# Kernel optimization log

Measured on AMD Instinct MI355X. Metric: run time of the kernel, lower is better.

Reference implementation:

```python
import jax, jax.numpy as jnp
import numpy as np

K = 121          # kernel_size
C = 3            # channels
PAD = (K - 1) // 2  # 60, replicate padding so output matches input spatial size


def setup_inputs() -> dict:
    key = jax.random.key(0)
    k1, k2 = jax.random.split(key)
    x = jax.random.normal(k1, (8, C, 512, 512), dtype=jnp.float32)
    sigma = jax.random.uniform(k2, (), dtype=jnp.float32)
    return {"x": x, "sigma": sigma}


def _gaussian_kernel(sigma):
    # sigma -> sigma*8 + 16, variance = sigma**2 (as in torch forward)
    s = sigma * 8.0 + 16.0
    variance = s * s
    coord = jnp.arange(K, dtype=jnp.float32) - (K - 1) / 2.0  # centered coords
    diff = -(coord[:, None] ** 2 + coord[None, :] ** 2)       # [K,K], -((x-m)^2+(y-m)^2)
    kern = jnp.exp(diff / (2.0 * variance))
    # the 1/(2*pi*variance) prefactor cancels under normalization
    kern = kern / jnp.sum(kern)
    return kern


def reference(x, sigma):
    kern = _gaussian_kernel(sigma)
    # depthwise weights: [out_ch=C, in_ch/groups=1, K, K]
    w = jnp.broadcast_to(kern[None, None, :, :], (C, 1, K, K))
    # replicate padding (torch 'replicate' == jnp 'edge')
    xp = jnp.pad(x, ((0, 0), (0, 0), (PAD, PAD), (PAD, PAD)), mode="edge")
    out = jax.lax.conv_general_dilated(
        xp, w,
        window_strides=(1, 1),
        padding="VALID",
        dimension_numbers=("NCHW", "OIHW", "NCHW"),
        feature_group_count=C,
    )
    return out
```

## Files before the change

kernel.cpp:

```cpp
#include <hip/hip_runtime.h>


#define HH    512
#define WW    512
#define PLANE (512 * 512)
#define NIMG  24
#define SROW  960

__device__ __forceinline__ int qla(int s) {
    return 10 * (s >> 2) + 2 * (s & 3);
}

__device__ __forceinline__ void make_weights(const float* __restrict__ sigma,
                                             float* __restrict__ wlds, int tid) {
    const float s = sigma[0] * 8.0f + 16.0f;
    const float inv2v = 1.0f / (2.0f * s * s);
    const int lane = tid & 63;
    const float c1 = (float)lane - 60.0f;
    float sum = __expf(-c1 * c1 * inv2v);
    if (lane + 64 <= 120) {
        const float c2 = (float)(lane + 64) - 60.0f;
        sum += __expf(-c2 * c2 * inv2v);
    }
    #pragma unroll
    for (int off = 1; off < 64; off <<= 1) sum += __shfl_xor(sum, off);
    if (tid < 128) {
        float g = 0.0f;
        if (tid <= 120) {
            const float c = (float)tid - 60.0f;
            g = __expf(-c * c * inv2v);
        }
        wlds[tid] = g / sum;
    }
}

#define V_OCT(CUR, NXT, KO)                                               \
    { *(float4*)&wq[0] = *(const float4*)&wlds[(KO) * 8];                 \
      *(float4*)&wq[4] = *(const float4*)&wlds[(KO) * 8 + 4];             \
      _Pragma("unroll")                                                   \
      for (int ki = 0; ki < 8; ++ki) {                                    \
          int rr = r0 - 52 + (KO) * 8 + ki;                               \
          rr = rr < 0 ? 0 : (rr > HH - 1 ? HH - 1 : rr);                  \
          NXT[ki] = *(const float2*)&src[(size_t)rr * WW];                \
          const float wk = wq[ki];                                        \
          _Pragma("unroll")                                               \
          for (int j = 0; j < 8; ++j) {                                   \
              const int idx = ki + j;                                     \
              const float2 v = (idx < 8) ? CUR[idx] : NXT[idx - 8];       \
              vac[j].x += wk * v.x; vac[j].y += wk * v.y;                 \
          }                                                               \
      }                                                                   \
    }

#define LOADW(DST, MB)                                                    \
    { const int F = 20 * (L + (MB));                                      \
      const float4 A = *(const float4*)&bs[F];                            \
      const float4 Bq = *(const float4*)&bs[F + 4];                       \
      const float4 Cq = *(const float4*)&bs[F + 10];                      \
      const float4 Dq = *(const float4*)&bs[F + 14];                      \
      DST[0] = make_float2(A.x, A.y);   DST[1] = make_float2(A.z, A.w);   \
      DST[2] = make_float2(Bq.x, Bq.y); DST[3] = make_float2(Bq.z, Bq.w); \
      DST[4] = make_float2(Cq.x, Cq.y); DST[5] = make_float2(Cq.z, Cq.w); \
      DST[6] = make_float2(Dq.x, Dq.y); DST[7] = make_float2(Dq.z, Dq.w); }

#define H_OCT(CUR, NXT, KO)                                               \
    { LOADW(NXT, (KO) + 1)                                                \
      *(float4*)&wq[0] = *(const float4*)&wlds[(KO) * 8];                 \
      *(float4*)&wq[4] = *(const float4*)&wlds[(KO) * 8 + 4];             \
      _Pragma("unroll")                                                   \
      for (int ki = 0; ki < 8; ++ki) {                                    \
          const float wk = wq[ki];                                        \
          _Pragma("unroll")                                               \
          for (int j = 0; j < 8; ++j) {                                   \
              const int idx = ki + j;                                     \
              const float2 v = (idx < 8) ? CUR[idx] : NXT[idx - 8];       \
              hac[j].x += wk * v.x; hac[j].y += wk * v.y;                 \
          }                                                               \
      }                                                                   \
    }

__global__ __launch_bounds__(256, 5) void blur_fused(
        const float* __restrict__ x, const float* __restrict__ sigma,
        float* __restrict__ out) {
    __shared__ float sm[8 * SROW];
    __shared__ float wlds[128];
    const int tid = threadIdx.x;

    const int lid   = blockIdx.x + gridDim.x * blockIdx.y;
    const int tile  = (lid & 7) * 192 + (lid >> 3);
    const int r0    = (tile & 63) * 8;
    const int plane = tile >> 6;

    const int c0 = tid * 2;
    const float* __restrict__ src = x + (size_t)plane * PLANE + c0;

    float2 wa[8], wb[8], vac[8];
    float  wq[8];
    #pragma unroll
    for (int m = 0; m < 8; ++m) {
        int rr = r0 - 60 + m;
        rr = rr < 0 ? 0 : rr;
        wa[m] = *(const float2*)&src[(size_t)rr * WW];
    }
    make_weights(sigma, wlds, tid);
    #pragma unroll
    for (int j = 0; j < 8; ++j) vac[j] = make_float2(0.f, 0.f);
    __syncthreads();

    #pragma unroll 1
    for (int ko = 0; ko < 16; ko += 2) {
        V_OCT(wa, wb, ko)
        V_OCT(wb, wa, ko + 1)
    }

    {
        const int laX0 = qla(c0 + 60), laX1 = qla(c0 + 61);
        const int laY0 = qla(c0 - 196) + 1, laY1 = qla(c0 - 195) + 1;
        #pragma unroll
        for (int j = 0; j < 8; ++j) {
            float* rp = sm + j * SROW;
            if (c0 < 324) { rp[laX0] = vac[j].x; rp[laX1] = vac[j].y; }
            if (c0 >= 196) { rp[laY0] = vac[j].x; rp[laY1] = vac[j].y; }
        }
    }
    if (tid < 64) {
        #pragma unroll
        for (int j = 0; j < 8; ++j) {
            const float lv = __shfl(vac[j].x, 0);
            if (tid < 60) sm[j * SROW + qla(tid)] = lv;
        }
    } else if (tid >= 192) {
        const int l = tid & 63;
        #pragma unroll
        for (int j = 0; j < 8; ++j) {
            const float rv = __shfl(vac[j].y, 63);
            sm[j * SROW + qla(316 + l) + 1] = rv;
            if (l < 4) sm[j * SROW + qla(380 + l) + 1] = rv;
        }
    }
    __syncthreads();

    const int r = tid >> 5;
    const int L = tid & 31;
    const float* __restrict__ bs = sm + r * SROW;

    float2 ha[8], hb[8], hac[8];
    #pragma unroll
    for (int j = 0; j < 8; ++j) hac[j] = make_float2(0.f, 0.f);

    LOADW(ha, 0)

    #pragma unroll 1
    for (int ko = 0; ko < 16; ko += 2) {
        H_OCT(ha, hb, ko)
        H_OCT(hb, ha, ko + 1)
    }

    float* __restrict__ dst = out + (size_t)plane * PLANE
                                  + (size_t)(r0 + r) * WW + L * 8;
    *(float4*)(dst)       = make_float4(hac[0].x, hac[1].x, hac[2].x, hac[3].x);
    *(float4*)(dst + 4)   = make_float4(hac[4].x, hac[5].x, hac[6].x, hac[7].x);
    *(float4*)(dst + 256) = make_float4(hac[0].y, hac[1].y, hac[2].y, hac[3].y);
    *(float4*)(dst + 260) = make_float4(hac[4].y, hac[5].y, hac[6].y, hac[7].y);
}

extern "C" void kernel_launch(void* const* d_in, const int* in_sizes, int n_in,
                              void* d_out, int out_size, void* d_ws, size_t ws_size,
                              hipStream_t stream) {
    const float* x     = (const float*)d_in[0];
    const float* sigma = (const float*)d_in[1];
    float* out = (float*)d_out;
    blur_fused<<<dim3(HH / 8, NIMG), dim3(256), 0, stream>>>(x, sigma, out);
}
```

Baseline: 119.6 us.

## Use packed FP32 FMA and triple-buffer row/column windows for deeper prefetch

Replaces scalar FMAs with inline v_pk_fma_f32 on duplicated float2 weights, which halves the FMA instruction count in both vertical and horizontal passes. Adds a third register buffer so loads run two octets ahead of use, giving more latency hiding. Occupancy hint drops from 5 to 4 blocks per CU to make room for the extra registers. Weights in LDS are stored as float2 pairs, doubling weight LDS traffic, and the shared buffer is padded.

```diff
diff --git a/kernel.cpp b/kernel.cpp
--- a/kernel.cpp
+++ b/kernel.cpp
@@ -12,7 +12,7 @@
 }
 
 __device__ __forceinline__ void make_weights(const float* __restrict__ sigma,
-                                             float* __restrict__ wlds, int tid) {
+                                             float2* __restrict__ wlds2, int tid) {
     const float s = sigma[0] * 8.0f + 16.0f;
     const float inv2v = 1.0f / (2.0f * s * s);
     const int lane = tid & 63;
@@ -30,24 +30,36 @@
             const float c = (float)tid - 60.0f;
             g = __expf(-c * c * inv2v);
         }
-        wlds[tid] = g / sum;
+        const float gn = g / sum;
+        wlds2[tid] = make_float2(gn, gn);
     }
 }
 
-#define V_OCT(CUR, NXT, KO)                                               \
-    { *(float4*)&wq[0] = *(const float4*)&wlds[(KO) * 8];                 \
-      *(float4*)&wq[4] = *(const float4*)&wlds[(KO) * 8 + 4];             \
+#define LOADWQ(KO)                                                        \
+    *(float4*)&wq2[0] = *(const float4*)&wlds2[(KO) * 8];                 \
+    *(float4*)&wq2[2] = *(const float4*)&wlds2[(KO) * 8 + 2];             \
+    *(float4*)&wq2[4] = *(const float4*)&wlds2[(KO) * 8 + 4];             \
+    *(float4*)&wq2[6] = *(const float4*)&wlds2[(KO) * 8 + 6];
+
+#define PKFMA(ACC, V, W)                                                  \
+    asm("v_pk_fma_f32 %0, %1, %2, %0" : "+v"(ACC) : "v"(V), "v"(W));
+
+#define V_OCT(W0, W1, W2, KO)                                             \
+    { _Pragma("unroll")                                                   \
+      for (int ki = 0; ki < 8; ++ki) {                                    \
+          int rr = r0 - 60 + ((KO) + 2) * 8 + ki;                         \
+          rr = rr < 0 ? 0 : (rr > HH - 1 ? HH - 1 : rr);                  \
+          W2[ki] = *(const float2*)&src[(size_t)rr * WW];                 \
+      }                                                                   \
+      LOADWQ(KO)                                                          \
       _Pragma("unroll")                                                   \
       for (int ki = 0; ki < 8; ++ki) {                                    \
-          int rr = r0 - 52 + (KO) * 8 + ki;                               \
-          rr = rr < 0 ? 0 : (rr > HH - 1 ? HH - 1 : rr);                  \
-          NXT[ki] = *(const float2*)&src[(size_t)rr * WW];                \
-          const float wk = wq[ki];                                        \
+          const float2 wk2 = wq2[ki];                                     \
           _Pragma("unroll")                                               \
           for (int j = 0; j < 8; ++j) {                                   \
               const int idx = ki + j;                                     \
-              const float2 v = (idx < 8) ? CUR[idx] : NXT[idx - 8];       \
-              vac[j].x += wk * v.x; vac[j].y += wk * v.y;                 \
+              const float2 v = (idx < 8) ? W0[idx] : W1[idx - 8];         \
+              PKFMA(vac[j], v, wk2)                                       \
           }                                                               \
       }                                                                   \
     }
@@ -63,27 +75,26 @@
       DST[4] = make_float2(Cq.x, Cq.y); DST[5] = make_float2(Cq.z, Cq.w); \
       DST[6] = make_float2(Dq.x, Dq.y); DST[7] = make_float2(Dq.z, Dq.w); }
 
-#define H_OCT(CUR, NXT, KO)                                               \
-    { LOADW(NXT, (KO) + 1)                                                \
-      *(float4*)&wq[0] = *(const float4*)&wlds[(KO) * 8];                 \
-      *(float4*)&wq[4] = *(const float4*)&wlds[(KO) * 8 + 4];             \
+#define H_OCT(W0, W1, W2, KO)                                             \
+    { LOADW(W2, (KO) + 2)                                                 \
+      LOADWQ(KO)                                                          \
       _Pragma("unroll")                                                   \
       for (int ki = 0; ki < 8; ++ki) {                                    \
-          const float wk = wq[ki];                                        \
+          const float2 wk2 = wq2[ki];                                     \
           _Pragma("unroll")                                               \
           for (int j = 0; j < 8; ++j) {                                   \
               const int idx = ki + j;                                     \
-              const float2 v = (idx < 8) ? CUR[idx] : NXT[idx - 8];       \
-              hac[j].x += wk * v.x; hac[j].y += wk * v.y;                 \
+              const float2 v = (idx < 8) ? W0[idx] : W1[idx - 8];         \
+              PKFMA(hac[j], v, wk2)                                       \
           }                                                               \
       }                                                                   \
     }
 
-__global__ __launch_bounds__(256, 5) void blur_fused(
+__global__ __launch_bounds__(256, 4) void blur_fused(
         const float* __restrict__ x, const float* __restrict__ sigma,
         float* __restrict__ out) {
-    __shared__ float sm[8 * SROW];
-    __shared__ float wlds[128];
+    __shared__ float  sm[8 * SROW + 40];
+    __shared__ float2 wlds2[128];
     const int tid = threadIdx.x;
 
     const int lid   = blockIdx.x + gridDim.x * blockIdx.y;
@@ -94,24 +105,31 @@
     const int c0 = tid * 2;
     const float* __restrict__ src = x + (size_t)plane * PLANE + c0;
 
-    float2 wa[8], wb[8], vac[8];
-    float  wq[8];
+    float2 Wa[8], Wb[8], Wc[8], vac[8], wq2[8];
     #pragma unroll
     for (int m = 0; m < 8; ++m) {
         int rr = r0 - 60 + m;
         rr = rr < 0 ? 0 : rr;
-        wa[m] = *(const float2*)&src[(size_t)rr * WW];
+        Wa[m] = *(const float2*)&src[(size_t)rr * WW];
     }
-    make_weights(sigma, wlds, tid);
+    #pragma unroll
+    for (int m = 0; m < 8; ++m) {
+        int rr = r0 - 52 + m;
+        rr = rr < 0 ? 0 : rr;
+        Wb[m] = *(const float2*)&src[(size_t)rr * WW];
+    }
+    make_weights(sigma, wlds2, tid);
     #pragma unroll
     for (int j = 0; j < 8; ++j) vac[j] = make_float2(0.f, 0.f);
     __syncthreads();
 
     #pragma unroll 1
-    for (int ko = 0; ko < 16; ko += 2) {
-        V_OCT(wa, wb, ko)
-        V_OCT(wb, wa, ko + 1)
+    for (int ko = 0; ko < 15; ko += 3) {
+        V_OCT(Wa, Wb, Wc, ko)
+        V_OCT(Wb, Wc, Wa, ko + 1)
+        V_OCT(Wc, Wa, Wb, ko + 2)
     }
+    V_OCT(Wa, Wb, Wc, 15)
 
     {
         const int laX0 = qla(c0 + 60), laX1 = qla(c0 + 61);
@@ -144,17 +162,20 @@
     const int L = tid & 31;
     const float* __restrict__ bs = sm + r * SROW;
 
-    float2 ha[8], hb[8], hac[8];
+    float2 Ha[8], Hb[8], Hc[8], hac[8];
     #pragma unroll
     for (int j = 0; j < 8; ++j) hac[j] = make_float2(0.f, 0.f);
 
-    LOADW(ha, 0)
+    LOADW(Ha, 0)
+    LOADW(Hb, 1)
 
     #pragma unroll 1
-    for (int ko = 0; ko < 16; ko += 2) {
-        H_OCT(ha, hb, ko)
-        H_OCT(hb, ha, ko + 1)
+    for (int ko = 0; ko < 15; ko += 3) {
+        H_OCT(Ha, Hb, Hc, ko)
+        H_OCT(Hb, Hc, Ha, ko + 1)
+        H_OCT(Hc, Ha, Hb, ko + 2)
     }
+    H_OCT(Ha, Hb, Hc, 15)
 
     float* __restrict__ dst = out + (size_t)plane * PLANE
                                   + (size_t)(r0 + r) * WW + L * 8;
```

Measured after the change: 121.3 us. No clear change (+1.3%).
